# Optimization experiments

Hardware: AMD Instinct MI355X
Metric: run time of the kernel (lower is better)

Reference implementation:

```python
import jax, jax.numpy as jnp
import numpy as np

HIDDEN = 50

def setup_inputs() -> dict:
    key = jax.random.key(0)
    ks = jax.random.split(key, 6)
    B, T, F = 4096, 200, 32
    x = jax.random.normal(ks[0], (B, T, F), dtype=jnp.float32)
    # SimpleRNN params (keras defaults: glorot_uniform kernel, orthogonal recurrent, zero bias)
    lim = np.sqrt(6.0 / (F + HIDDEN))
    W = jax.random.uniform(ks[1], (F, HIDDEN), minval=-lim, maxval=lim, dtype=jnp.float32)
    U = jnp.linalg.qr(jax.random.normal(ks[2], (HIDDEN, HIDDEN)))[0].astype(jnp.float32)
    b = jnp.zeros((HIDDEN,), dtype=jnp.float32)
    # Dense head: RandomNormal(stddev=0.01) kernel, zero bias
    Wd = 0.01 * jax.random.normal(ks[3], (HIDDEN, 1), dtype=jnp.float32)
    bd = jnp.zeros((1,), dtype=jnp.float32)
    return {"x": x, "W": W, "U": U, "b": b, "Wd": Wd, "bd": bd}

def reference(x, W, U, b, Wd, bd):
    B = x.shape[0]
    # Precompute input projections for all timesteps in one GEMM: [B,T,H]
    xw = jnp.einsum('btf,fh->bth', x, W) + b
    h0 = jnp.zeros((B, HIDDEN), dtype=x.dtype)

    def step(h, xw_t):
        h_new = jnp.tanh(xw_t + h @ U)
        return h_new, None

    h_last, _ = jax.lax.scan(step, h0, jnp.swapaxes(xw, 0, 1))  # scan over T
    return jax.nn.relu(h_last @ Wd + bd)  # [B, 1]
```

## Files before the change

### kernel.cpp

```cpp
#include <hip/hip_runtime.h>

#define TT 200
#define FF 32
#define HH 50
#define NCH 13

typedef _Float16 half8 __attribute__((ext_vector_type(8)));
typedef __attribute__((ext_vector_type(4))) float f32x4;
typedef __attribute__((ext_vector_type(4))) unsigned int uint32x4;

__device__ __forceinline__ float fast_tanh(float x) {
    float e = exp2f(2.885390082f * x);
    return fmaf(-2.0f, __builtin_amdgcn_rcpf(e + 1.0f), 1.0f);
}
__device__ __forceinline__ f32x4 mfmah(half8 a, half8 b, f32x4 c) {
    return __builtin_amdgcn_mfma_f32_16x16x32_f16(a, b, c, 0, 0, 0);
}

__device__ __forceinline__ half8 build_wfrag(const float* __restrict__ M, int kbase,
                                             int kmax, int c, bool cv, int g) {
    unsigned u[4];
#pragma unroll
    for (int q = 0; q < 4; ++q) {
        const int k0 = kbase + 8 * g + 2 * q, k1 = k0 + 1;
        _Float16 v0 = (_Float16)((cv && k0 < kmax) ? M[k0 * HH + c] : 0.0f);
        _Float16 v1 = (_Float16)((cv && k1 < kmax) ? M[k1 * HH + c] : 0.0f);
        u[q] = ((unsigned)__builtin_bit_cast(unsigned short, v1) << 16)
             |  __builtin_bit_cast(unsigned short, v0);
    }
    uint32x4 uu = {u[0], u[1], u[2], u[3]};
    return __builtin_bit_cast(half8, uu);
}

__device__ __forceinline__ half8 cvt8(float4 a, float4 b) {
    unsigned u0 = __builtin_bit_cast(unsigned, __builtin_amdgcn_cvt_pkrtz(a.x, a.y));
    unsigned u1 = __builtin_bit_cast(unsigned, __builtin_amdgcn_cvt_pkrtz(a.z, a.w));
    unsigned u2 = __builtin_bit_cast(unsigned, __builtin_amdgcn_cvt_pkrtz(b.x, b.y));
    unsigned u3 = __builtin_bit_cast(unsigned, __builtin_amdgcn_cvt_pkrtz(b.z, b.w));
    uint32x4 uu = {u0, u1, u2, u3};
    return __builtin_bit_cast(half8, uu);
}

__global__
__attribute__((amdgpu_flat_work_group_size(64, 64)))
__attribute__((amdgpu_waves_per_eu(2, 2)))
void rnn_fp16(const float* __restrict__ x, const float* __restrict__ W,
              const float* __restrict__ U, const float* __restrict__ b,
              const float* __restrict__ Wd, const float* __restrict__ bd,
              float* __restrict__ out)
{
    __shared__ float xw[2][16][2][64];
    __shared__ _Float16 hl[2][2][64];

    const int l = threadIdx.x & 63;
    const int r = l & 15;
    const int g = l >> 4;
    const int rl = r & 1;
    const int rb = blockIdx.x * 2;
    const bool gs1 = (g & 1) != 0, gs2 = (g & 2) != 0;
    const int cg = 16 * g + r;

    half8 Wf[4], U0[4], U1[4];
    f32x4 biasv[4];
#pragma unroll
    for (int n = 0; n < 4; ++n) {
        const int c = 16 * n + r;
        const bool cv = (c < HH);
        Wf[n] = build_wfrag(W, 0,  FF, c, cv, g);
        U0[n] = build_wfrag(U, 0,  HH, c, cv, g);
        U1[n] = build_wfrag(U, 32, HH, c, cv, g);
        const float bv = cv ? b[c] : 0.0f;
        biasv[n] = (f32x4){bv, bv, bv, bv};
    }
    const f32x4 kzero = {0.0f, 0.0f, 0.0f, 0.0f};
    const float wd = (cg < HH) ? Wd[cg] : 0.0f;

    const float* x0 = x + (size_t)(rb + 0) * TT * FF;
    const float* x1 = x + (size_t)(rb + 1) * TT * FF;

    float4 r0a, r0b, r1a, r1b;
    auto chunk_load = [&](int cc) {
        int tt = 16 * cc + r; if (tt > TT - 1) tt = TT - 1;
        const float* p0 = x0 + (size_t)tt * FF + 8 * g;
        const float* p1 = x1 + (size_t)tt * FF + 8 * g;
        r0a = *(const float4*)p0; r0b = *(const float4*)(p0 + 4);
        r1a = *(const float4*)p1; r1b = *(const float4*)(p1 + 4);
    };
    auto chunk_compute = [&](int cc) {
        half8 a0 = cvt8(r0a, r0b);
        half8 a1 = cvt8(r1a, r1b);
        const int par = cc & 1;
#pragma unroll
        for (int n = 0; n < 4; ++n) {
            f32x4 c0 = mfmah(a0, Wf[n], biasv[n]);
            f32x4 c1 = mfmah(a1, Wf[n], biasv[n]);
            asm volatile("" : "+v"(c0), "+v"(c1));
#pragma unroll
            for (int i = 0; i < 4; ++i) {
                xw[par][4 * g + i][0][16 * n + r] = c0[i];
                xw[par][4 * g + i][1][16 * n + r] = c1[i];
            }
        }
    };

    chunk_load(0);
    chunk_compute(0);
    chunk_load(1);
    ((unsigned*)hl)[l] = 0u;
    ((unsigned*)hl)[64 + l] = 0u;

    float hf0 = 0.0f, hf1 = 0.0f;

    for (int c = 0; c < NCH; ++c) {
        const float* xwp = (c & 1) ? &xw[1][0][0][cg] : &xw[0][0][0][cg];
        const int nsteps = (c == NCH - 1) ? (TT - 16 * (NCH - 1)) : 16;
#pragma unroll
        for (int tl = 0; tl < 16; ++tl) {
            if (tl >= nsteps) break;
            const int buf = tl & 1;
            const _Float16* hp = &hl[buf][rl][0];
            half8 A0 = *(const half8*)(hp + 8 * g);
            half8 A1 = *(const half8*)(hp + 32 + 8 * g);

            f32x4 tot[4];
#pragma unroll
            for (int n = 0; n < 4; ++n)
                tot[n] = mfmah(A1, U1[n], mfmah(A0, U0[n], kzero));
            asm volatile("" : "+v"(tot[0]), "+v"(tot[1]), "+v"(tot[2]), "+v"(tot[3]));

            if (tl == 8) {
                if (c + 1 < NCH) chunk_compute(c + 1);
                if (c + 2 < NCH) chunk_load(c + 2);
            }

            float a0 = gs1 ? tot[1][0] : tot[0][0];
            float a1 = gs1 ? tot[1][1] : tot[0][1];
            float c0 = gs1 ? tot[3][0] : tot[2][0];
            float c1 = gs1 ? tot[3][1] : tot[2][1];
            float m0 = gs2 ? c0 : a0;
            float m1 = gs2 ? c1 : a1;
            m0 += xwp[tl * 128];
            m1 += xwp[tl * 128 + 64];
            hf0 = fast_tanh(m0);
            hf1 = fast_tanh(m1);
            hl[buf ^ 1][0][cg] = (_Float16)hf0;
            hl[buf ^ 1][1][cg] = (_Float16)hf1;
        }
    }

    float p0 = hf0 * wd, p1 = hf1 * wd;
#pragma unroll
    for (int m = 1; m <= 32; m <<= 1) {
        p0 += __shfl_xor(p0, m);
        p1 += __shfl_xor(p1, m);
    }
    if (l == 0) {
        const float bdv = bd[0];
        out[rb + 0] = fmaxf(p0 + bdv, 0.0f);
        out[rb + 1] = fmaxf(p1 + bdv, 0.0f);
    }
}

extern "C" void kernel_launch(void* const* d_in, const int* in_sizes, int n_in,
                              void* d_out, int out_size, void* d_ws, size_t ws_size,
                              hipStream_t stream) {
    const float* x  = (const float*)d_in[0];
    const float* W  = (const float*)d_in[1];
    const float* U  = (const float*)d_in[2];
    const float* b  = (const float*)d_in[3];
    const float* Wd = (const float*)d_in[4];
    const float* bd = (const float*)d_in[5];
    float* out = (float*)d_out;
    const int B = out_size;
    dim3 grid(B / 2), block(64);
    hipLaunchKernelGGL(rnn_fp16, grid, block, 0, stream,
                       x, W, U, b, Wd, bd, out);
    (void)d_ws; (void)ws_size; (void)in_sizes; (void)n_in;
}
```

Measured before the change: 65.17 us.

## Process four batch rows per wavefront instead of two in the RNN recurrence

Each 64-lane wavefront now carries four batch rows through the recurrence instead of two, packing pairs of fp16 hidden states into 32-bit LDS words and unpacking them with byte permutes to build the MFMA A operands. This uses more of the 16-row MFMA tile per serial timestep and halves the grid, so each step's MFMA and tanh latency covers more work. In exchange each step adds LDS reads and permute instructions, the x staging buffer doubles, and waves_per_eu drops to 1, which lowers per-EU occupancy and latency hiding.

```diff
diff --git a/kernel.cpp b/kernel.cpp
--- a/kernel.cpp
+++ b/kernel.cpp
@@ -43,22 +43,23 @@
 
 __global__
 __attribute__((amdgpu_flat_work_group_size(64, 64)))
-__attribute__((amdgpu_waves_per_eu(2, 2)))
+__attribute__((amdgpu_waves_per_eu(1, 1)))
 void rnn_fp16(const float* __restrict__ x, const float* __restrict__ W,
               const float* __restrict__ U, const float* __restrict__ b,
               const float* __restrict__ Wd, const float* __restrict__ bd,
               float* __restrict__ out)
 {
-    __shared__ float xw[2][16][2][64];
-    __shared__ _Float16 hl[2][2][64];
-
-    const int l = threadIdx.x & 63;
-    const int r = l & 15;
-    const int g = l >> 4;
-    const int rl = r & 1;
-    const int rb = blockIdx.x * 2;
+    __shared__ float xw[2][16][4][64];
+    __shared__ unsigned hl[2][2][64];
+
+    const int l  = threadIdx.x & 63;
+    const int r  = l & 15;
+    const int g  = l >> 4;
+    const int rp = (r & 3) >> 1;
+    const int rb = blockIdx.x * 4;
     const bool gs1 = (g & 1) != 0, gs2 = (g & 2) != 0;
-    const int cg = 16 * g + r;
+    const int cg = l;
+    const unsigned psel = (r & 1) ? 0x07060302u : 0x05040100u;
 
     half8 Wf[4], U0[4], U1[4];
     f32x4 biasv[4];
@@ -75,30 +76,40 @@
     const f32x4 kzero = {0.0f, 0.0f, 0.0f, 0.0f};
     const float wd = (cg < HH) ? Wd[cg] : 0.0f;
 
-    const float* x0 = x + (size_t)(rb + 0) * TT * FF;
-    const float* x1 = x + (size_t)(rb + 1) * TT * FF;
-
-    float4 r0a, r0b, r1a, r1b;
+    const float* xr0 = x + (size_t)(rb + 0) * TT * FF;
+    const float* xr1 = x + (size_t)(rb + 1) * TT * FF;
+    const float* xr2 = x + (size_t)(rb + 2) * TT * FF;
+    const float* xr3 = x + (size_t)(rb + 3) * TT * FF;
+
+    float4 s0a, s0b, s1a, s1b, s2a, s2b, s3a, s3b;
     auto chunk_load = [&](int cc) {
         int tt = 16 * cc + r; if (tt > TT - 1) tt = TT - 1;
-        const float* p0 = x0 + (size_t)tt * FF + 8 * g;
-        const float* p1 = x1 + (size_t)tt * FF + 8 * g;
-        r0a = *(const float4*)p0; r0b = *(const float4*)(p0 + 4);
-        r1a = *(const float4*)p1; r1b = *(const float4*)(p1 + 4);
+        const float* p0 = xr0 + (size_t)tt * FF + 8 * g;
+        const float* p1 = xr1 + (size_t)tt * FF + 8 * g;
+        const float* p2 = xr2 + (size_t)tt * FF + 8 * g;
+        const float* p3 = xr3 + (size_t)tt * FF + 8 * g;
+        s0a = *(const float4*)p0; s0b = *(const float4*)(p0 + 4);
+        s1a = *(const float4*)p1; s1b = *(const float4*)(p1 + 4);
+        s2a = *(const float4*)p2; s2b = *(const float4*)(p2 + 4);
+        s3a = *(const float4*)p3; s3b = *(const float4*)(p3 + 4);
     };
     auto chunk_compute = [&](int cc) {
-        half8 a0 = cvt8(r0a, r0b);
-        half8 a1 = cvt8(r1a, r1b);
+        half8 a0 = cvt8(s0a, s0b), a1 = cvt8(s1a, s1b);
+        half8 a2 = cvt8(s2a, s2b), a3 = cvt8(s3a, s3b);
         const int par = cc & 1;
 #pragma unroll
         for (int n = 0; n < 4; ++n) {
             f32x4 c0 = mfmah(a0, Wf[n], biasv[n]);
             f32x4 c1 = mfmah(a1, Wf[n], biasv[n]);
-            asm volatile("" : "+v"(c0), "+v"(c1));
+            f32x4 c2 = mfmah(a2, Wf[n], biasv[n]);
+            f32x4 c3 = mfmah(a3, Wf[n], biasv[n]);
 #pragma unroll
             for (int i = 0; i < 4; ++i) {
-                xw[par][4 * g + i][0][16 * n + r] = c0[i];
-                xw[par][4 * g + i][1][16 * n + r] = c1[i];
+                float* q = &xw[par][4 * g + i][0][16 * n + r];
+                q[0]   = c0[i];
+                q[64]  = c1[i];
+                q[128] = c2[i];
+                q[192] = c3[i];
             }
         }
     };
@@ -106,58 +117,79 @@
     chunk_load(0);
     chunk_compute(0);
     chunk_load(1);
-    ((unsigned*)hl)[l] = 0u;
-    ((unsigned*)hl)[64 + l] = 0u;
-
-    float hf0 = 0.0f, hf1 = 0.0f;
+    hl[0][0][l] = 0u;
+    hl[0][1][l] = 0u;
+
+    float h0 = 0.0f, h1 = 0.0f, h2 = 0.0f, h3 = 0.0f;
 
     for (int c = 0; c < NCH; ++c) {
-        const float* xwp = (c & 1) ? &xw[1][0][0][cg] : &xw[0][0][0][cg];
+        const int par = c & 1;
         const int nsteps = (c == NCH - 1) ? (TT - 16 * (NCH - 1)) : 16;
 #pragma unroll
         for (int tl = 0; tl < 16; ++tl) {
             if (tl >= nsteps) break;
             const int buf = tl & 1;
-            const _Float16* hp = &hl[buf][rl][0];
-            half8 A0 = *(const half8*)(hp + 8 * g);
-            half8 A1 = *(const half8*)(hp + 32 + 8 * g);
+            const unsigned* hp = &hl[buf][rp][0];
+            uint32x4 w0 = *(const uint32x4*)(hp + 8 * g);
+            uint32x4 w1 = *(const uint32x4*)(hp + 8 * g + 4);
+            uint32x4 w2 = *(const uint32x4*)(hp + 32 + 8 * g);
+            uint32x4 w3 = *(const uint32x4*)(hp + 32 + 8 * g + 4);
+            uint32x4 pa = {__builtin_amdgcn_perm(w0[1], w0[0], psel),
+                           __builtin_amdgcn_perm(w0[3], w0[2], psel),
+                           __builtin_amdgcn_perm(w1[1], w1[0], psel),
+                           __builtin_amdgcn_perm(w1[3], w1[2], psel)};
+            uint32x4 pb = {__builtin_amdgcn_perm(w2[1], w2[0], psel),
+                           __builtin_amdgcn_perm(w2[3], w2[2], psel),
+                           __builtin_amdgcn_perm(w3[1], w3[0], psel),
+                           __builtin_amdgcn_perm(w3[3], w3[2], psel)};
+            half8 A0 = __builtin_bit_cast(half8, pa);
+            half8 A1 = __builtin_bit_cast(half8, pb);
 
             f32x4 tot[4];
 #pragma unroll
             for (int n = 0; n < 4; ++n)
                 tot[n] = mfmah(A1, U1[n], mfmah(A0, U0[n], kzero));
-            asm volatile("" : "+v"(tot[0]), "+v"(tot[1]), "+v"(tot[2]), "+v"(tot[3]));
 
             if (tl == 8) {
                 if (c + 1 < NCH) chunk_compute(c + 1);
                 if (c + 2 < NCH) chunk_load(c + 2);
             }
 
-            float a0 = gs1 ? tot[1][0] : tot[0][0];
-            float a1 = gs1 ? tot[1][1] : tot[0][1];
-            float c0 = gs1 ? tot[3][0] : tot[2][0];
-            float c1 = gs1 ? tot[3][1] : tot[2][1];
-            float m0 = gs2 ? c0 : a0;
-            float m1 = gs2 ? c1 : a1;
-            m0 += xwp[tl * 128];
-            m1 += xwp[tl * 128 + 64];
-            hf0 = fast_tanh(m0);
-            hf1 = fast_tanh(m1);
-            hl[buf ^ 1][0][cg] = (_Float16)hf0;
-            hl[buf ^ 1][1][cg] = (_Float16)hf1;
+            float m0 = gs2 ? (gs1 ? tot[3][0] : tot[2][0]) : (gs1 ? tot[1][0] : tot[0][0]);
+            float m1 = gs2 ? (gs1 ? tot[3][1] : tot[2][1]) : (gs1 ? tot[1][1] : tot[0][1]);
+            float m2 = gs2 ? (gs1 ? tot[3][2] : tot[2][2]) : (gs1 ? tot[1][2] : tot[0][2]);
+            float m3 = gs2 ? (gs1 ? tot[3][3] : tot[2][3]) : (gs1 ? tot[1][3] : tot[0][3]);
+
+            const float* xq = &xw[par][tl][0][cg];
+            m0 += xq[0];
+            m1 += xq[64];
+            m2 += xq[128];
+            m3 += xq[192];
+            h0 = fast_tanh(m0);
+            h1 = fast_tanh(m1);
+            h2 = fast_tanh(m2);
+            h3 = fast_tanh(m3);
+            hl[buf ^ 1][0][cg] = __builtin_bit_cast(unsigned,
+                __builtin_amdgcn_cvt_pkrtz(h0, h1));
+            hl[buf ^ 1][1][cg] = __builtin_bit_cast(unsigned,
+                __builtin_amdgcn_cvt_pkrtz(h2, h3));
         }
     }
 
-    float p0 = hf0 * wd, p1 = hf1 * wd;
+    float p0 = h0 * wd, p1 = h1 * wd, p2 = h2 * wd, p3 = h3 * wd;
 #pragma unroll
     for (int m = 1; m <= 32; m <<= 1) {
         p0 += __shfl_xor(p0, m);
         p1 += __shfl_xor(p1, m);
+        p2 += __shfl_xor(p2, m);
+        p3 += __shfl_xor(p3, m);
     }
     if (l == 0) {
         const float bdv = bd[0];
         out[rb + 0] = fmaxf(p0 + bdv, 0.0f);
         out[rb + 1] = fmaxf(p1 + bdv, 0.0f);
+        out[rb + 2] = fmaxf(p2 + bdv, 0.0f);
+        out[rb + 3] = fmaxf(p3 + bdv, 0.0f);
     }
 }
 
@@ -172,7 +204,7 @@
     const float* bd = (const float*)d_in[5];
     float* out = (float*)d_out;
     const int B = out_size;
-    dim3 grid(B / 2), block(64);
+    dim3 grid(B / 4), block(64);
     hipLaunchKernelGGL(rnn_fp16, grid, block, 0, stream,
                        x, W, U, b, Wd, bd, out);
     (void)d_ws; (void)ws_size; (void)in_sizes; (void)n_in;
```

Result: slower. 85.55 us (+31.3%).
